# Performance work log

Hardware: AMD Instinct MI355X
Metric: run time of the kernel (lower is better)

The kernel has to match this reference:

```python
import jax, jax.numpy as jnp
import numpy as np

EPS = 1e-5

def setup_inputs() -> dict:
    key = jax.random.key(0)
    B, N, F_in, F_out = 8, 2048, 64, 64
    ks = jax.random.split(key, 8)
    batch_nb_nodes = jax.random.randint(ks[0], (B,), N // 2, N + 1).astype(jnp.int32)
    node_mask = (jnp.arange(N)[None, :] < batch_nb_nodes[:, None]).astype(jnp.float32)  # [B,N]
    adj_mask = node_mask[:, :, None] * node_mask[:, None, :]                            # [B,N,N]
    emb_in = jax.random.normal(ks[1], (B, N, F_in), jnp.float32) * node_mask[:, :, None]
    adj_in = jax.random.uniform(ks[2], (B, N, N), jnp.float32) * adj_mask
    kernel_sigma = jnp.asarray(float(F_in), jnp.float32)          # gaussian kernel bandwidth
    combine_w = jnp.array([0.5, 0.5], jnp.float32)                # affine combine of [adj_in, kernel]
    conv_W = jax.random.normal(ks[3], (2 * F_in, F_out), jnp.float32) / np.float32(np.sqrt(2 * F_in))
    conv_b = jnp.zeros((F_out,), jnp.float32)
    nu_W = jax.random.normal(ks[4], (F_in + F_out, F_out), jnp.float32) / np.float32(np.sqrt(F_in + F_out))
    nu_b = jnp.zeros((F_out,), jnp.float32)
    return {"emb_in": emb_in, "adj_in": adj_in, "adj_mask": adj_mask,
            "batch_nb_nodes": batch_nb_nodes, "kernel_sigma": kernel_sigma,
            "combine_w": combine_w, "conv_W": conv_W, "conv_b": conv_b,
            "nu_W": nu_W, "nu_b": nu_b}

def reference(emb_in, adj_in, adj_mask, batch_nb_nodes, kernel_sigma, combine_w, conv_W, conv_b, nu_W, nu_b):
    B, N, F = emb_in.shape
    # --- gaussian kernel adjacency update: K_ij = exp(-||e_i - e_j||^2 / sigma) ---
    sq = jnp.sum(emb_in * emb_in, axis=-1)                                  # [B,N]
    d2 = sq[:, :, None] + sq[:, None, :] - 2.0 * jnp.einsum('bif,bjf->bij', emb_in, emb_in)
    ker = jnp.exp(-jnp.maximum(d2, 0.0) / kernel_sigma)                     # [B,N,N]
    # --- affine combine of previous adjacency and kernel matrices, then mask ---
    adj = (combine_w[0] * adj_in + combine_w[1] * ker) * adj_mask           # [B,N,N]
    # --- spatialnorm: per-graph mean/std over valid nodes (layer_nb != 0) ---
    node_mask = (jnp.arange(N)[None, :] < batch_nb_nodes[:, None]).astype(emb_in.dtype)  # [B,N]
    cnt = jnp.maximum(batch_nb_nodes.astype(emb_in.dtype), 1.0)[:, None, None]
    m = node_mask[:, :, None]
    mean = jnp.sum(emb_in * m, axis=1, keepdims=True) / cnt                 # [B,1,F]
    var = jnp.sum(((emb_in - mean) ** 2) * m, axis=1, keepdims=True) / cnt  # [B,1,F]
    emb_n = ((emb_in - mean) / jnp.sqrt(var + EPS)) * m                     # mask_embedding
    # --- operators: degree (D @ x) and adjacency (A @ x), joined then conv ---
    deg = jnp.sum(adj, axis=-1)                                             # [B,N]
    op_deg = deg[:, :, None] * emb_n                                        # [B,N,F]
    op_adj = jnp.einsum('bij,bjf->bif', adj, emb_n)                         # [B,N,F]
    emb_upd = jnp.concatenate([op_deg, op_adj], axis=-1) @ conv_W + conv_b  # [B,N,F_out]
    # --- node update: relu(W [emb_in ; emb_update] + b) ---
    emb = jax.nn.relu(jnp.concatenate([emb_in, emb_upd], axis=-1) @ nu_W + nu_b)
    return emb, adj
```

## Files before the change

kernel.cpp:

```cpp
#include <hip/hip_runtime.h>
#include <math.h>

#define BB 8
#define NN 2048
#define FF 64
#define EPSV 1e-5f
#define EMB_SZ (BB * NN * FF)

#define WS_SQ      0
#define WS_ASUM    (BB * NN)
#define WS_ASQ     (WS_ASUM + BB * FF)
#define WS_MEAN    (WS_ASQ + BB * FF)
#define WS_RSTD    (WS_MEAN + BB * FF)
#define WS_DEG     (WS_RSTD + BB * FF)
#define WS_F32_END (WS_DEG + BB * NN)

typedef __attribute__((ext_vector_type(8))) short bf16x8;
typedef __attribute__((ext_vector_type(4))) float f32x4;
typedef unsigned short ushort_t;

__device__ inline ushort_t f2bf(float x) {
    union { float f; unsigned u; } v; v.f = x;
    return (ushort_t)((v.u + 0x7fffu + ((v.u >> 16) & 1u)) >> 16);
}

__global__ __launch_bounds__(256) void k_stats(const float* __restrict__ emb,
                                               float* __restrict__ sq,
                                               float* __restrict__ asum,
                                               float* __restrict__ asq) {
    const int b    = blockIdx.y;
    const int lane = threadIdx.x & 63;
    const int grp  = threadIdx.x >> 6;
    const int base_i = blockIdx.x << 6;

    float s = 0.f, q = 0.f;
    for (int it = 0; it < 16; ++it) {
        const int i = base_i + (it << 2) + grp;
        const float x = emb[((size_t)(b * NN + i) << 6) + lane];
        const float x2 = x * x;
        s += x;
        q += x2;
        float r = x2;
        r += __shfl_xor(r, 1);
        r += __shfl_xor(r, 2);
        r += __shfl_xor(r, 4);
        r += __shfl_xor(r, 8);
        r += __shfl_xor(r, 16);
        r += __shfl_xor(r, 32);
        if (lane == 0) sq[b * NN + i] = r;
    }
    __shared__ float redS[4][64];
    __shared__ float redQ[4][64];
    redS[grp][lane] = s;
    redQ[grp][lane] = q;
    __syncthreads();
    if (threadIdx.x < 64) {
        const float ts = redS[0][lane] + redS[1][lane] + redS[2][lane] + redS[3][lane];
        const float tq = redQ[0][lane] + redQ[1][lane] + redQ[2][lane] + redQ[3][lane];
        atomicAdd(&asum[(b << 6) + lane], ts);
        atomicAdd(&asq[(b << 6) + lane], tq);
    }
}

__global__ void k_finalize(const float* __restrict__ asum, const float* __restrict__ asq,
                           const int* __restrict__ nbp,
                           float* __restrict__ mean, float* __restrict__ rstd) {
    const int t = threadIdx.x;
    const int b = t >> 6;
    const float cnt = fmaxf((float)nbp[b], 1.f);
    const float m = asum[t] / cnt;
    float v = asq[t] / cnt - m * m;
    v = fmaxf(v, 0.f);
    mean[t] = m;
    rstd[t] = rsqrtf(v + EPSV);
}

__global__ __launch_bounds__(256) void k_prep(const float* __restrict__ emb,
                                              const float* __restrict__ meanp,
                                              const float* __restrict__ rstdp,
                                              const int* __restrict__ nbp,
                                              ushort_t* __restrict__ embBf,
                                              ushort_t* __restrict__ embnT) {
    __shared__ __align__(16) ushort_t T[64][72];
    const int b = blockIdx.y, j0 = blockIdx.x << 6;
    const int nb = nbp[b], bN = b * NN;
    const int t = threadIdx.x;
    const int j = t >> 2, fs = (t & 3) << 4;

    float mn[16], rs[16];
#pragma unroll
    for (int e = 0; e < 16; e += 4) {
        *(float4*)&mn[e] = *(const float4*)(meanp + (b << 6) + fs + e);
        *(float4*)&rs[e] = *(const float4*)(rstdp + (b << 6) + fs + e);
    }
    const float msk = (j0 + j < nb) ? 1.f : 0.f;
    const float* src = emb + ((size_t)(bN + j0 + j) << 6) + fs;
    __align__(16) float x[16];
    *(float4*)(x + 0)  = *(const float4*)(src + 0);
    *(float4*)(x + 4)  = *(const float4*)(src + 4);
    *(float4*)(x + 8)  = *(const float4*)(src + 8);
    *(float4*)(x + 12) = *(const float4*)(src + 12);
    __align__(16) ushort_t raw[16];
#pragma unroll
    for (int e = 0; e < 16; ++e) {
        raw[e] = f2bf(x[e]);
        T[fs + e][j] = f2bf((x[e] - mn[e]) * rs[e] * msk);
    }
    ushort_t* dst = embBf + ((size_t)(bN + j0 + j) << 6) + fs;
    *(bf16x8*)dst       = *(bf16x8*)&raw[0];
    *(bf16x8*)(dst + 8) = *(bf16x8*)&raw[8];
    __syncthreads();
    const int f = t >> 2, js = (t & 3) << 4;
    const bf16x8 v0 = *(bf16x8*)&T[f][js];
    const bf16x8 v1 = *(bf16x8*)&T[f][js + 8];
    ushort_t* dstT = embnT + ((size_t)(b * FF + f) << 11) + j0 + js;
    *(bf16x8*)dstT       = v0;
    *(bf16x8*)(dstT + 8) = v1;
}

__global__ __launch_bounds__(256, 4) void k_adj_deg(const ushort_t* __restrict__ embBf,
                                                    const float* __restrict__ adj_in,
                                                    const float* __restrict__ sq,
                                                    const float* __restrict__ sigp,
                                                    const float* __restrict__ cw,
                                                    const int* __restrict__ nbp,
                                                    float* __restrict__ adj_out,
                                                    float* __restrict__ deg) {
    const int b = blockIdx.z, i0 = blockIdx.y << 6, j0 = blockIdx.x << 7;
    const int nb = nbp[b], bN = b * NN;
    const int tid = threadIdx.x, w = tid >> 6, lane = tid & 63;
    const int l15 = lane & 15, lq = lane >> 4;

    if (i0 >= nb || j0 >= nb) {
        const float4 z = make_float4(0.f, 0.f, 0.f, 0.f);
#pragma unroll
        for (int q = 0; q < 8; ++q) {
            const int idx = (tid << 3) + q;
            const int row = idx >> 5, c4 = (idx & 31) << 2;
            *(float4*)(adj_out + ((size_t)(bN + i0 + row) << 11) + j0 + c4) = z;
        }
        return;
    }

    const int ib = i0 + w * 16;

    float ain[4][8];
#pragma unroll
    for (int r = 0; r < 4; ++r) {
        const float* arow = adj_in + ((size_t)(bN + ib + lq * 4 + r) << 11) + j0 + l15;
#pragma unroll
        for (int c = 0; c < 8; ++c) ain[r][c] = arow[c << 4];
    }
    float sqi[4], sqj[8];
#pragma unroll
    for (int r = 0; r < 4; ++r) sqi[r] = sq[bN + ib + lq * 4 + r];
#pragma unroll
    for (int c = 0; c < 8; ++c) sqj[c] = sq[bN + j0 + c * 16 + l15];

    const ushort_t* ap = embBf + ((size_t)(bN + ib + l15) << 6) + lq * 8;
    const bf16x8 a0 = *(const bf16x8*)ap;
    const bf16x8 a1 = *(const bf16x8*)(ap + 32);

    f32x4 acc[8];
#pragma unroll
    for (int c = 0; c < 8; ++c) acc[c] = (f32x4){0.f, 0.f, 0.f, 0.f};
#pragma unroll
    for (int c = 0; c < 8; ++c) {
        const ushort_t* bp = embBf + ((size_t)(bN + j0 + c * 16 + l15) << 6) + lq * 8;
        const bf16x8 b0 = *(const bf16x8*)bp;
        const bf16x8 b1 = *(const bf16x8*)(bp + 32);
        acc[c] = __builtin_amdgcn_mfma_f32_16x16x32_bf16(a0, b0, acc[c], 0, 0, 0);
        acc[c] = __builtin_amdgcn_mfma_f32_16x16x32_bf16(a1, b1, acc[c], 0, 0, 0);
    }

    const float inv_sigma = 1.0f / sigp[0];
    const float w0 = cw[0], w1 = cw[1];
#pragma unroll
    for (int r = 0; r < 4; ++r) {
        const int gi = ib + lq * 4 + r;
        const float mi = (gi < nb) ? 1.f : 0.f;
        float* orow = adj_out + ((size_t)(bN + gi) << 11) + j0 + l15;
        float rsum = 0.f;
#pragma unroll
        for (int c = 0; c < 8; ++c) {
            const int gj = j0 + c * 16 + l15;
            float d2 = sqi[r] + sqj[c] - 2.f * acc[c][r];
            d2 = fmaxf(d2, 0.f);
            const float ker = __expf(-d2 * inv_sigma);
            const float mv = (gj < nb) ? mi : 0.f;
            const float o = (w0 * ain[r][c] + w1 * ker) * mv;
            orow[c << 4] = o;
            rsum += o;
        }
        rsum += __shfl_xor(rsum, 1);
        rsum += __shfl_xor(rsum, 2);
        rsum += __shfl_xor(rsum, 4);
        rsum += __shfl_xor(rsum, 8);
        if (l15 == 0) atomicAdd(&deg[bN + gi], rsum);
    }
}

__global__ __launch_bounds__(256, 4) void k_opadj(const float* __restrict__ adj,
                                                  const ushort_t* __restrict__ embnT,
                                                  const int* __restrict__ nbp,
                                                  float* __restrict__ opadj) {
    const int b = blockIdx.z, i0 = blockIdx.x << 6, jbeg = blockIdx.y << 9;
    const int nb = nbp[b];
    if (i0 >= nb || jbeg >= nb) return;
    const int bN = b * NN;
    const int jend = min(jbeg + 512, (nb + 31) & ~31);

    const int tid = threadIdx.x, w = tid >> 6, lane = tid & 63;
    const int l15 = lane & 15, lq = lane >> 4;

    const float* arow = adj + ((size_t)(bN + i0 + w * 16 + l15) << 11);
    const ushort_t* bbase = embnT + ((size_t)(b * FF + l15) << 11);

    f32x4 acc[4];
#pragma unroll
    for (int c = 0; c < 4; ++c) acc[c] = (f32x4){0.f, 0.f, 0.f, 0.f};

    for (int jt = jbeg; jt < jend; jt += 32) {
        const float* ap = arow + jt + lq * 8;
        const float4 x0 = *(const float4*)ap;
        const float4 x1 = *(const float4*)(ap + 4);
        __align__(16) ushort_t af[8];
        af[0] = f2bf(x0.x); af[1] = f2bf(x0.y); af[2] = f2bf(x0.z); af[3] = f2bf(x0.w);
        af[4] = f2bf(x1.x); af[5] = f2bf(x1.y); af[6] = f2bf(x1.z); af[7] = f2bf(x1.w);
        const bf16x8 a = *(bf16x8*)af;
#pragma unroll
        for (int c = 0; c < 4; ++c) {
            const bf16x8 bv = *(const bf16x8*)(bbase + ((size_t)(c * 16) << 11) + jt + lq * 8);
            acc[c] = __builtin_amdgcn_mfma_f32_16x16x32_bf16(a, bv, acc[c], 0, 0, 0);
        }
    }

#pragma unroll
    for (int c = 0; c < 4; ++c)
#pragma unroll
        for (int r = 0; r < 4; ++r) {
            const int gi = i0 + w * 16 + lq * 4 + r;
            atomicAdd(opadj + ((size_t)(bN + gi) << 6) + c * 16 + l15, acc[c][r]);
        }
}

__global__ __launch_bounds__(256) void k_epilogue(const float* __restrict__ emb,
                                                  const float* __restrict__ meanp,
                                                  const float* __restrict__ rstdp,
                                                  const float* __restrict__ degp,
                                                  const int* __restrict__ nbp,
                                                  const float* __restrict__ convW,
                                                  const float* __restrict__ convB,
                                                  const float* __restrict__ nuW,
                                                  const float* __restrict__ nuB,
                                                  float* __restrict__ emb_out) {
    __shared__ __align__(16) float smem[13056];
    float* xs = smem;
    float* us = smem + 8704;
    float* es = smem;

    const int b   = blockIdx.y;
    const int i0  = blockIdx.x << 6;
    const int tid = threadIdx.x;
    const int tx = tid & 15, ty = tid >> 4;
    const int nb = nbp[b];
    const int bN = b * NN;
    const int sj  = tid >> 2;
    const int scb = (tid & 3) << 4;

    {
        const float4 m4 = *(const float4*)(meanp + (b << 6) + (tx << 2));
        const float4 r4 = *(const float4*)(rstdp + (b << 6) + (tx << 2));
#pragma unroll
        for (int u = 0; u < 4; ++u) {
            const int il = (ty << 2) + u;
            const int gi = i0 + il;
            const float msk = (gi < nb) ? 1.f : 0.f;
            const float dg = degp[bN + gi];
            const float4 v = *(const float4*)(emb + ((size_t)(bN + gi) << 6) + (tx << 2));
            float4 en;
            en.x = (v.x - m4.x) * r4.x * msk;
            en.y = (v.y - m4.y) * r4.y * msk;
            en.z = (v.z - m4.z) * r4.z * msk;
            en.w = (v.w - m4.w) * r4.w * msk;
            float4 od;
            od.x = dg * en.x; od.y = dg * en.y; od.z = dg * en.z; od.w = dg * en.w;
            *(float4*)&xs[il * 132 + (tx << 2)] = od;
            const float4 oa = *(const float4*)(emb_out + ((size_t)(bN + gi) << 6) + (tx << 2));
            *(float4*)&xs[il * 132 + 64 + (tx << 2)] = oa;
        }
    }
    __syncthreads();

    {
        float u4[4][4];
#pragma unroll
        for (int r = 0; r < 4; ++r)
#pragma unroll
            for (int c = 0; c < 4; ++c) u4[r][c] = 0.f;
        for (int fis = 0; fis < 128; fis += 4) {
            const float4 w0v = *(const float4*)(convW + ((fis + 0) << 6) + (tx << 2));
            const float4 w1v = *(const float4*)(convW + ((fis + 1) << 6) + (tx << 2));
            const float4 w2v = *(const float4*)(convW + ((fis + 2) << 6) + (tx << 2));
            const float4 w3v = *(const float4*)(convW + ((fis + 3) << 6) + (tx << 2));
#pragma unroll
            for (int r = 0; r < 4; ++r) {
                const float4 x = *(const float4*)&xs[((ty << 2) + r) * 132 + fis];
                u4[r][0] += x.x * w0v.x + x.y * w1v.x + x.z * w2v.x + x.w * w3v.x;
                u4[r][1] += x.x * w0v.y + x.y * w1v.y + x.z * w2v.y + x.w * w3v.y;
                u4[r][2] += x.x * w0v.z + x.y * w1v.z + x.z * w2v.z + x.w * w3v.z;
                u4[r][3] += x.x * w0v.w + x.y * w1v.w + x.z * w2v.w + x.w * w3v.w;
            }
        }
        const float4 cb4 = *(const float4*)(convB + (tx << 2));
#pragma unroll
        for (int r = 0; r < 4; ++r) {
            float4 o;
            o.x = u4[r][0] + cb4.x; o.y = u4[r][1] + cb4.y;
            o.z = u4[r][2] + cb4.z; o.w = u4[r][3] + cb4.w;
            *(float4*)&us[((ty << 2) + r) * 68 + (tx << 2)] = o;
        }
    }
    __syncthreads();

    {
        const float* pe = emb + ((size_t)(bN + i0 + sj) << 6) + scb;
#pragma unroll
        for (int u = 0; u < 4; ++u)
            *(float4*)&es[sj * 68 + scb + (u << 2)] = *(const float4*)(pe + (u << 2));
    }
    __syncthreads();

    {
        float u4[4][4];
#pragma unroll
        for (int r = 0; r < 4; ++r)
#pragma unroll
            for (int c = 0; c < 4; ++c) u4[r][c] = 0.f;
        for (int fis = 0; fis < 64; fis += 4) {
            const float4 w0v = *(const float4*)(nuW + ((fis + 0) << 6) + (tx << 2));
            const float4 w1v = *(const float4*)(nuW + ((fis + 1) << 6) + (tx << 2));
            const float4 w2v = *(const float4*)(nuW + ((fis + 2) << 6) + (tx << 2));
            const float4 w3v = *(const float4*)(nuW + ((fis + 3) << 6) + (tx << 2));
#pragma unroll
            for (int r = 0; r < 4; ++r) {
                const float4 x = *(const float4*)&es[((ty << 2) + r) * 68 + fis];
                u4[r][0] += x.x * w0v.x + x.y * w1v.x + x.z * w2v.x + x.w * w3v.x;
                u4[r][1] += x.x * w0v.y + x.y * w1v.y + x.z * w2v.y + x.w * w3v.y;
                u4[r][2] += x.x * w0v.z + x.y * w1v.z + x.z * w2v.z + x.w * w3v.z;
                u4[r][3] += x.x * w0v.w + x.y * w1v.w + x.z * w2v.w + x.w * w3v.w;
            }
        }
        for (int fis = 0; fis < 64; fis += 4) {
            const float4 w0v = *(const float4*)(nuW + ((64 + fis + 0) << 6) + (tx << 2));
            const float4 w1v = *(const float4*)(nuW + ((64 + fis + 1) << 6) + (tx << 2));
            const float4 w2v = *(const float4*)(nuW + ((64 + fis + 2) << 6) + (tx << 2));
            const float4 w3v = *(const float4*)(nuW + ((64 + fis + 3) << 6) + (tx << 2));
#pragma unroll
            for (int r = 0; r < 4; ++r) {
                const float4 x = *(const float4*)&us[((ty << 2) + r) * 68 + fis];
                u4[r][0] += x.x * w0v.x + x.y * w1v.x + x.z * w2v.x + x.w * w3v.x;
                u4[r][1] += x.x * w0v.y + x.y * w1v.y + x.z * w2v.y + x.w * w3v.y;
                u4[r][2] += x.x * w0v.z + x.y * w1v.z + x.z * w2v.z + x.w * w3v.z;
                u4[r][3] += x.x * w0v.w + x.y * w1v.w + x.z * w2v.w + x.w * w3v.w;
            }
        }
        const float4 nb4 = *(const float4*)(nuB + (tx << 2));
#pragma unroll
        for (int r = 0; r < 4; ++r) {
            const int gi = i0 + (ty << 2) + r;
            float4 o;
            o.x = fmaxf(u4[r][0] + nb4.x, 0.f);
            o.y = fmaxf(u4[r][1] + nb4.y, 0.f);
            o.z = fmaxf(u4[r][2] + nb4.z, 0.f);
            o.w = fmaxf(u4[r][3] + nb4.w, 0.f);
            *(float4*)(emb_out + ((size_t)(bN + gi) << 6) + (tx << 2)) = o;
        }
    }
}

extern "C" void kernel_launch(void* const* d_in, const int* in_sizes, int n_in,
                              void* d_out, int out_size, void* d_ws, size_t ws_size,
                              hipStream_t stream) {
    (void)in_sizes; (void)n_in; (void)out_size; (void)ws_size;
    const float* emb_in   = (const float*)d_in[0];
    const float* adj_in   = (const float*)d_in[1];
    const int*   nbp      = (const int*)d_in[3];
    const float* sigp     = (const float*)d_in[4];
    const float* cw       = (const float*)d_in[5];
    const float* convW    = (const float*)d_in[6];
    const float* convB    = (const float*)d_in[7];
    const float* nuW      = (const float*)d_in[8];
    const float* nuB      = (const float*)d_in[9];

    float* emb_out = (float*)d_out;
    float* adj_out = (float*)d_out + EMB_SZ;

    float* ws   = (float*)d_ws;
    float* sq   = ws + WS_SQ;
    float* asum = ws + WS_ASUM;
    float* asq  = ws + WS_ASQ;
    float* mean = ws + WS_MEAN;
    float* rstd = ws + WS_RSTD;
    float* deg  = ws + WS_DEG;
    ushort_t* embBf = (ushort_t*)(ws + WS_F32_END);
    ushort_t* embnT = embBf + (size_t)BB * NN * FF;

    hipMemsetAsync(asum, 0, (WS_F32_END - WS_ASUM) * sizeof(float), stream);
    hipMemsetAsync(emb_out, 0, (size_t)EMB_SZ * sizeof(float), stream);

    k_stats<<<dim3(32, BB), 256, 0, stream>>>(emb_in, sq, asum, asq);
    k_finalize<<<1, BB * FF, 0, stream>>>(asum, asq, nbp, mean, rstd);
    k_prep<<<dim3(32, BB), 256, 0, stream>>>(emb_in, mean, rstd, nbp, embBf, embnT);
    k_adj_deg<<<dim3(NN / 128, NN / 64, BB), 256, 0, stream>>>(embBf, adj_in, sq, sigp,
                                                               cw, nbp, adj_out, deg);
    k_opadj<<<dim3(NN / 64, 4, BB), 256, 0, stream>>>(adj_out, embnT, nbp, emb_out);
    k_epilogue<<<dim3(32, BB), 256, 0, stream>>>(emb_in, mean, rstd, deg, nbp,
                                                 convW, convB, nuW, nuB, emb_out);
}
```

Measured before the change: 409.6 us.

## Fuse adjacency construction, degree, and A@emb_n matmul into one kernel

Merges the kernel that builds the combined adjacency and degree with the kernel that multiplies adjacency by the normalized embeddings. Each block now computes a 64x256 adjacency tile, writes it out, and stages it in LDS as bf16 for an immediate MFMA with the transposed embeddings. This removes the second full read of the 134 MB adjacency from global memory. LDS is also used to transpose the distance dot products so adj_in loads and adj_out stores become row-contiguous float4 accesses. In exchange it adds LDS usage, lowers the occupancy target to 3, and issues more atomics on the op_adj accumulator because the j-split is finer.

After: 414.2 us. Within noise of the previous version (+1.1%).

```diff
diff --git a/kernel.cpp b/kernel.cpp
--- a/kernel.cpp
+++ b/kernel.cpp
@@ -18,6 +18,9 @@
 typedef __attribute__((ext_vector_type(8))) short bf16x8;
 typedef __attribute__((ext_vector_type(4))) float f32x4;
 typedef unsigned short ushort_t;
+
+#define P1 132
+#define P2 136
 
 __device__ inline ushort_t f2bf(float x) {
     union { float f; unsigned u; } v; v.f = x;
@@ -118,130 +121,140 @@
     *(bf16x8*)(dstT + 8) = v1;
 }
 
-__global__ __launch_bounds__(256, 4) void k_adj_deg(const ushort_t* __restrict__ embBf,
-                                                    const float* __restrict__ adj_in,
-                                                    const float* __restrict__ sq,
-                                                    const float* __restrict__ sigp,
-                                                    const float* __restrict__ cw,
-                                                    const int* __restrict__ nbp,
-                                                    float* __restrict__ adj_out,
-                                                    float* __restrict__ deg) {
-    const int b = blockIdx.z, i0 = blockIdx.y << 6, j0 = blockIdx.x << 7;
+__global__ __launch_bounds__(256, 3) void k_adj_fused(const ushort_t* __restrict__ embBf,
+                                                      const ushort_t* __restrict__ embnT,
+                                                      const float* __restrict__ adj_in,
+                                                      const float* __restrict__ sq,
+                                                      const float* __restrict__ sigp,
+                                                      const float* __restrict__ cw,
+                                                      const int* __restrict__ nbp,
+                                                      float* __restrict__ adj_out,
+                                                      float* __restrict__ deg,
+                                                      float* __restrict__ opadj) {
+    __shared__ __align__(16) float    ldsF[4][16 * P1];
+    __shared__ __align__(16) ushort_t ldsH[4][16 * P2];
+
+    const int b = blockIdx.z, i0 = blockIdx.y << 6, jbeg = blockIdx.x << 8;
     const int nb = nbp[b], bN = b * NN;
     const int tid = threadIdx.x, w = tid >> 6, lane = tid & 63;
     const int l15 = lane & 15, lq = lane >> 4;
-
-    if (i0 >= nb || j0 >= nb) {
-        const float4 z = make_float4(0.f, 0.f, 0.f, 0.f);
-#pragma unroll
-        for (int q = 0; q < 8; ++q) {
-            const int idx = (tid << 3) + q;
-            const int row = idx >> 5, c4 = (idx & 31) << 2;
-            *(float4*)(adj_out + ((size_t)(bN + i0 + row) << 11) + j0 + c4) = z;
-        }
-        return;
-    }
-
     const int ib = i0 + w * 16;
-
-    float ain[4][8];
-#pragma unroll
-    for (int r = 0; r < 4; ++r) {
-        const float* arow = adj_in + ((size_t)(bN + ib + lq * 4 + r) << 11) + j0 + l15;
-#pragma unroll
-        for (int c = 0; c < 8; ++c) ain[r][c] = arow[c << 4];
-    }
-    float sqi[4], sqj[8];
-#pragma unroll
-    for (int r = 0; r < 4; ++r) sqi[r] = sq[bN + ib + lq * 4 + r];
-#pragma unroll
-    for (int c = 0; c < 8; ++c) sqj[c] = sq[bN + j0 + c * 16 + l15];
-
-    const ushort_t* ap = embBf + ((size_t)(bN + ib + l15) << 6) + lq * 8;
-    const bf16x8 a0 = *(const bf16x8*)ap;
-    const bf16x8 a1 = *(const bf16x8*)(ap + 32);
-
-    f32x4 acc[8];
-#pragma unroll
-    for (int c = 0; c < 8; ++c) acc[c] = (f32x4){0.f, 0.f, 0.f, 0.f};
-#pragma unroll
-    for (int c = 0; c < 8; ++c) {
-        const ushort_t* bp = embBf + ((size_t)(bN + j0 + c * 16 + l15) << 6) + lq * 8;
-        const bf16x8 b0 = *(const bf16x8*)bp;
-        const bf16x8 b1 = *(const bf16x8*)(bp + 32);
-        acc[c] = __builtin_amdgcn_mfma_f32_16x16x32_bf16(a0, b0, acc[c], 0, 0, 0);
-        acc[c] = __builtin_amdgcn_mfma_f32_16x16x32_bf16(a1, b1, acc[c], 0, 0, 0);
-    }
-
-    const float inv_sigma = 1.0f / sigp[0];
+    const int rrow = lane >> 2;
+    const int rcol = (lane & 3) << 5;
+
+    float*    ldsf = ldsF[w];
+    ushort_t* ldsh = ldsH[w];
+
+    const float inv_sigma = 1.f / sigp[0];
     const float w0 = cw[0], w1 = cw[1];
-#pragma unroll
-    for (int r = 0; r < 4; ++r) {
-        const int gi = ib + lq * 4 + r;
-        const float mi = (gi < nb) ? 1.f : 0.f;
-        float* orow = adj_out + ((size_t)(bN + gi) << 11) + j0 + l15;
+    const bool ilive = (i0 < nb);
+
+    bf16x8 a0 = {}, a1 = {};
+    float sqi_r = 0.f, mi_r = 0.f;
+    if (ilive) {
+        const ushort_t* ap = embBf + ((size_t)(bN + ib + l15) << 6) + lq * 8;
+        a0 = *(const bf16x8*)ap;
+        a1 = *(const bf16x8*)(ap + 32);
+        sqi_r = sq[bN + ib + rrow];
+        mi_r = (ib + rrow < nb) ? 1.f : 0.f;
+    }
+
+    f32x4 accP[4];
+#pragma unroll
+    for (int c = 0; c < 4; ++c) accP[c] = (f32x4){0.f, 0.f, 0.f, 0.f};
+
+    for (int t = 0; t < 2; ++t) {
+        const int j0 = jbeg + (t << 7);
+        float* orow = adj_out + ((size_t)(bN + ib + rrow) << 11) + j0 + rcol;
+
+        if (!ilive || j0 >= nb) {
+            const float4 z = make_float4(0.f, 0.f, 0.f, 0.f);
+#pragma unroll
+            for (int e = 0; e < 8; ++e) *(float4*)(orow + (e << 2)) = z;
+            continue;
+        }
+
+        float4 ain[8], sqj4[8];
+        const float* arow_in = adj_in + ((size_t)(bN + ib + rrow) << 11) + j0 + rcol;
+#pragma unroll
+        for (int e = 0; e < 8; ++e) ain[e] = *(const float4*)(arow_in + (e << 2));
+#pragma unroll
+        for (int e = 0; e < 8; ++e) sqj4[e] = *(const float4*)(sq + bN + j0 + rcol + (e << 2));
+
+        f32x4 acc[8];
+#pragma unroll
+        for (int c = 0; c < 8; ++c) acc[c] = (f32x4){0.f, 0.f, 0.f, 0.f};
+#pragma unroll
+        for (int c = 0; c < 8; ++c) {
+            const ushort_t* bp = embBf + ((size_t)(bN + j0 + c * 16 + l15) << 6) + lq * 8;
+            const bf16x8 b0 = *(const bf16x8*)bp;
+            const bf16x8 b1 = *(const bf16x8*)(bp + 32);
+            acc[c] = __builtin_amdgcn_mfma_f32_16x16x32_bf16(a0, b0, acc[c], 0, 0, 0);
+            acc[c] = __builtin_amdgcn_mfma_f32_16x16x32_bf16(a1, b1, acc[c], 0, 0, 0);
+        }
+
+#pragma unroll
+        for (int c = 0; c < 8; ++c)
+#pragma unroll
+            for (int r = 0; r < 4; ++r)
+                ldsf[(lq * 4 + r) * P1 + c * 16 + l15] = acc[c][r];
+
         float rsum = 0.f;
-#pragma unroll
-        for (int c = 0; c < 8; ++c) {
-            const int gj = j0 + c * 16 + l15;
-            float d2 = sqi[r] + sqj[c] - 2.f * acc[c][r];
-            d2 = fmaxf(d2, 0.f);
-            const float ker = __expf(-d2 * inv_sigma);
-            const float mv = (gj < nb) ? mi : 0.f;
-            const float o = (w0 * ain[r][c] + w1 * ker) * mv;
-            orow[c << 4] = o;
-            rsum += o;
-        }
+        float4 aout[8];
+#pragma unroll
+        for (int e = 0; e < 8; ++e) {
+            const float4 dot = *(const float4*)&ldsf[rrow * P1 + rcol + (e << 2)];
+            const int gj = j0 + rcol + (e << 2);
+            float4 o;
+            {
+                float d2 = fmaxf(sqi_r + sqj4[e].x - 2.f * dot.x, 0.f);
+                o.x = (w0 * ain[e].x + w1 * __expf(-d2 * inv_sigma)) * ((gj + 0 < nb) ? mi_r : 0.f);
+                d2 = fmaxf(sqi_r + sqj4[e].y - 2.f * dot.y, 0.f);
+                o.y = (w0 * ain[e].y + w1 * __expf(-d2 * inv_sigma)) * ((gj + 1 < nb) ? mi_r : 0.f);
+                d2 = fmaxf(sqi_r + sqj4[e].z - 2.f * dot.z, 0.f);
+                o.z = (w0 * ain[e].z + w1 * __expf(-d2 * inv_sigma)) * ((gj + 2 < nb) ? mi_r : 0.f);
+                d2 = fmaxf(sqi_r + sqj4[e].w - 2.f * dot.w, 0.f);
+                o.w = (w0 * ain[e].w + w1 * __expf(-d2 * inv_sigma)) * ((gj + 3 < nb) ? mi_r : 0.f);
+            }
+            aout[e] = o;
+            rsum += o.x + o.y + o.z + o.w;
+            *(float4*)(orow + (e << 2)) = o;
+        }
+
         rsum += __shfl_xor(rsum, 1);
         rsum += __shfl_xor(rsum, 2);
-        rsum += __shfl_xor(rsum, 4);
-        rsum += __shfl_xor(rsum, 8);
-        if (l15 == 0) atomicAdd(&deg[bN + gi], rsum);
-    }
-}
-
-__global__ __launch_bounds__(256, 4) void k_opadj(const float* __restrict__ adj,
-                                                  const ushort_t* __restrict__ embnT,
-                                                  const int* __restrict__ nbp,
-                                                  float* __restrict__ opadj) {
-    const int b = blockIdx.z, i0 = blockIdx.x << 6, jbeg = blockIdx.y << 9;
-    const int nb = nbp[b];
-    if (i0 >= nb || jbeg >= nb) return;
-    const int bN = b * NN;
-    const int jend = min(jbeg + 512, (nb + 31) & ~31);
-
-    const int tid = threadIdx.x, w = tid >> 6, lane = tid & 63;
-    const int l15 = lane & 15, lq = lane >> 4;
-
-    const float* arow = adj + ((size_t)(bN + i0 + w * 16 + l15) << 11);
-    const ushort_t* bbase = embnT + ((size_t)(b * FF + l15) << 11);
-
-    f32x4 acc[4];
-#pragma unroll
-    for (int c = 0; c < 4; ++c) acc[c] = (f32x4){0.f, 0.f, 0.f, 0.f};
-
-    for (int jt = jbeg; jt < jend; jt += 32) {
-        const float* ap = arow + jt + lq * 8;
-        const float4 x0 = *(const float4*)ap;
-        const float4 x1 = *(const float4*)(ap + 4);
-        __align__(16) ushort_t af[8];
-        af[0] = f2bf(x0.x); af[1] = f2bf(x0.y); af[2] = f2bf(x0.z); af[3] = f2bf(x0.w);
-        af[4] = f2bf(x1.x); af[5] = f2bf(x1.y); af[6] = f2bf(x1.z); af[7] = f2bf(x1.w);
-        const bf16x8 a = *(bf16x8*)af;
-#pragma unroll
-        for (int c = 0; c < 4; ++c) {
-            const bf16x8 bv = *(const bf16x8*)(bbase + ((size_t)(c * 16) << 11) + jt + lq * 8);
-            acc[c] = __builtin_amdgcn_mfma_f32_16x16x32_bf16(a, bv, acc[c], 0, 0, 0);
-        }
-    }
-
-#pragma unroll
-    for (int c = 0; c < 4; ++c)
-#pragma unroll
-        for (int r = 0; r < 4; ++r) {
-            const int gi = i0 + w * 16 + lq * 4 + r;
-            atomicAdd(opadj + ((size_t)(bN + gi) << 6) + c * 16 + l15, acc[c][r]);
-        }
+        if ((lane & 3) == 0) atomicAdd(&deg[bN + ib + rrow], rsum);
+
+#pragma unroll
+        for (int e2 = 0; e2 < 4; ++e2) {
+            __align__(16) ushort_t pk[8];
+            const float4 u = aout[e2 * 2], v = aout[e2 * 2 + 1];
+            pk[0] = f2bf(u.x); pk[1] = f2bf(u.y); pk[2] = f2bf(u.z); pk[3] = f2bf(u.w);
+            pk[4] = f2bf(v.x); pk[5] = f2bf(v.y); pk[6] = f2bf(v.z); pk[7] = f2bf(v.w);
+            *(bf16x8*)&ldsh[rrow * P2 + rcol + (e2 << 3)] = *(bf16x8*)pk;
+        }
+
+#pragma unroll
+        for (int ks = 0; ks < 4; ++ks) {
+            const bf16x8 af = *(const bf16x8*)&ldsh[l15 * P2 + ks * 32 + lq * 8];
+#pragma unroll
+            for (int c = 0; c < 4; ++c) {
+                const bf16x8 bv = *(const bf16x8*)(embnT + ((size_t)(b * FF + c * 16 + l15) << 11)
+                                                   + j0 + ks * 32 + lq * 8);
+                accP[c] = __builtin_amdgcn_mfma_f32_16x16x32_bf16(af, bv, accP[c], 0, 0, 0);
+            }
+        }
+    }
+
+    if (ilive) {
+#pragma unroll
+        for (int c = 0; c < 4; ++c)
+#pragma unroll
+            for (int r = 0; r < 4; ++r) {
+                const int gi = ib + lq * 4 + r;
+                atomicAdd(opadj + ((size_t)(bN + gi) << 6) + c * 16 + l15, accP[c][r]);
+            }
+    }
 }
 
 __global__ __launch_bounds__(256) void k_epilogue(const float* __restrict__ emb,
@@ -412,9 +425,9 @@
     k_stats<<<dim3(32, BB), 256, 0, stream>>>(emb_in, sq, asum, asq);
     k_finalize<<<1, BB * FF, 0, stream>>>(asum, asq, nbp, mean, rstd);
     k_prep<<<dim3(32, BB), 256, 0, stream>>>(emb_in, mean, rstd, nbp, embBf, embnT);
-    k_adj_deg<<<dim3(NN / 128, NN / 64, BB), 256, 0, stream>>>(embBf, adj_in, sq, sigp,
-                                                               cw, nbp, adj_out, deg);
-    k_opadj<<<dim3(NN / 64, 4, BB), 256, 0, stream>>>(adj_out, embnT, nbp, emb_out);
+    k_adj_fused<<<dim3(NN / 256, NN / 64, BB), 256, 0, stream>>>(embBf, embnT, adj_in,
+                                                                 sq, sigp, cw, nbp,
+                                                                 adj_out, deg, emb_out);
     k_epilogue<<<dim3(32, BB), 256, 0, stream>>>(emb_in, mean, rstd, deg, nbp,
                                                  convW, convB, nuW, nuB, emb_out);
 }
```
